# Kernel optimization log

Measured on AMD Instinct MI355X. Metric: run time of the kernel, lower is better.

The kernel has to match this reference:

```python
import jax, jax.numpy as jnp
import numpy as np

THRESHOLD = 0.05

def binarize101(w, threshold):
    # Ternary quantization to {-1, 0, +1}: zero inside the dead-zone [-thr, thr].
    pos = (w > threshold).astype(w.dtype)
    neg = (w < -threshold).astype(w.dtype)
    return pos - neg

def setup_inputs() -> dict:
    key = jax.random.key(0)
    k1, k2, k3 = jax.random.split(key, 3)
    x = jax.random.normal(k1, (8192, 4096), dtype=jnp.float32)
    weight = jax.random.normal(k2, (4096, 4096), dtype=jnp.float32)
    bias = jax.random.normal(k3, (4096,), dtype=jnp.float32)
    return {"x": x, "weight": weight, "bias": bias}

def reference(x, weight, bias):
    wb = binarize101(weight, THRESHOLD)
    # F.linear: x @ wb.T + bias ; x: [N, in], weight: [out, in] -> [N, out]
    return jnp.einsum('ni,oi->no', x, wb) + bias
```

## Files before the change

### kernel.cpp

```cpp
#include <hip/hip_runtime.h>

typedef float floatx16 __attribute__((ext_vector_type(16)));
typedef __bf16 bf16x8 __attribute__((ext_vector_type(8)));
using u16 = unsigned short;
using u32 = unsigned int;

#define GLOBAL_AS __attribute__((address_space(1)))
#define LDS_AS    __attribute__((address_space(3)))

__device__ __forceinline__ u32 rne_bf16(float f) {
  u32 u = __float_as_uint(f);
  return (u + 0x7FFFu + ((u >> 16) & 1u)) >> 16;
}

__global__ __launch_bounds__(256) void cvt_x_perm(const float* __restrict__ x,
                                                  u16* __restrict__ xb, int K) {
  __shared__ u16 sm[16384];
  const int tid = threadIdx.x;
  const int Kt = K >> 6;
  const int pn = blockIdx.x / Kt, tt = blockIdx.x % Kt;
  const float* src = x + (size_t)pn * 256 * K + tt * 64;
#pragma unroll
  for (int j = 0; j < 16; ++j) {
    const int fc = j * 256 + tid;
    const int row = fc >> 4, kl4 = fc & 15;
    const float4 v = *(const float4*)(src + (size_t)row * K + kl4 * 4);
    uint2 o;
    o.x = rne_bf16(v.x) | (rne_bf16(v.y) << 16);
    o.y = rne_bf16(v.z) | (rne_bf16(v.w) << 16);
    const int gi = row >> 5, rowin = row & 31;
    const int ks = kl4 >> 2;
    const int lane = rowin + 32 * ((kl4 >> 1) & 1);
    const int e4 = (kl4 & 1) * 4;
    *(uint2*)(sm + gi * 2048 + ks * 512 + lane * 8 + e4) = o;
  }
  __syncthreads();
  u16* dst = xb + (size_t)pn * 256 * K + (size_t)tt * 16384;
#pragma unroll
  for (int j = 0; j < 8; ++j) {
    const int o = (j * 256 + tid) * 8;
    *(uint4*)(dst + o) = *(const uint4*)(sm + o);
  }
}

__global__ __launch_bounds__(256) void quant_w_perm(const float* __restrict__ w,
                                                    u16* __restrict__ wb, int K) {
  __shared__ u16 sm[16384];
  const int tid = threadIdx.x;
  const int Kt = K >> 6;
  const int pn = blockIdx.x / Kt, tt = blockIdx.x % Kt;
  const float* src = w + (size_t)pn * 256 * K + tt * 64;
#pragma unroll
  for (int j = 0; j < 16; ++j) {
    const int fc = j * 256 + tid;
    const int row = fc >> 4, kl4 = fc & 15;
    const float4 v = *(const float4*)(src + (size_t)row * K + kl4 * 4);
    float vv[4] = {v.x, v.y, v.z, v.w};
    u32 r[4];
#pragma unroll
    for (int e = 0; e < 4; ++e)
      r[e] = (vv[e] > 0.05f) ? 0x3F80u : ((vv[e] < -0.05f) ? 0xBF80u : 0u);
    uint2 o;
    o.x = r[0] | (r[1] << 16);
    o.y = r[2] | (r[3] << 16);
    const int gi = row >> 5, rowin = row & 31;
    const int ks = kl4 >> 2;
    const int lane = rowin + 32 * ((kl4 >> 1) & 1);
    const int e4 = (kl4 & 1) * 4;
    *(uint2*)(sm + gi * 2048 + ks * 512 + lane * 8 + e4) = o;
  }
  __syncthreads();
  u16* dst = wb + (size_t)pn * 256 * K + (size_t)tt * 16384;
#pragma unroll
  for (int j = 0; j < 8; ++j) {
    const int o = (j * 256 + tid) * 8;
    *(uint4*)(dst + o) = *(const uint4*)(sm + o);
  }
}

__global__ __launch_bounds__(512, 2) void gemm_bin_m201d(
    const u16* __restrict__ Ap, const u16* __restrict__ Bp,
    const float* __restrict__ bias, float* __restrict__ C,
    int M, int N, int K) {
  __shared__ u16 lds[65536];

  const int tid = threadIdx.x;
  const int w = tid >> 6, l = tid & 63;
  const int wr = w >> 2, wc = w & 3;

  const int nbn = N >> 8;
  int wg = blockIdx.x;
  const int nwg = gridDim.x;
  if ((nwg & 7) == 0) wg = (wg & 7) * (nwg >> 3) + (wg >> 3);
  const int bm = wg / nbn, bn = wg % nbn;

  const int T = K >> 6;

  const u16* const Abase = Ap + (size_t)bm * ((size_t)K << 8) + tid * 8;
  const u16* const Bbase = Bp + (size_t)bn * ((size_t)K << 8) + tid * 8;

  const u16* const afp0 = lds + wr * 8192 + l * 8;
  const u16* const bfp0 = lds + 16384 + wc * 4096 + l * 8;

  floatx16 acc[4][2] = {};
  bf16x8 af[8], bflo[4], bfhi[4];

#define GLOAD(gptr, u16off)                                                    \
  __builtin_amdgcn_global_load_lds((const GLOBAL_AS void*)(gptr),              \
                                   (LDS_AS void*)(lds + (u16off)), 16, 0, 0)
#define BARRIER __builtin_amdgcn_s_barrier()
#define LGKM0  do { asm volatile("s_waitcnt lgkmcnt(0)" ::: "memory");         \
                    __builtin_amdgcn_sched_barrier(0); } while (0)

  GLOAD(Abase + 0 * 4096,      0 + tid * 8);
  GLOAD(Abase + 2 * 4096,   8192 + tid * 8);
  GLOAD(Bbase + 0 * 4096,  16384 + tid * 8);
  GLOAD(Bbase + 1 * 4096,  20480 + tid * 8);
  GLOAD(Bbase + 2 * 4096,  24576 + tid * 8);
  GLOAD(Bbase + 3 * 4096,  28672 + tid * 8);
  GLOAD(Abase + 1 * 4096,   4096 + tid * 8);
  GLOAD(Abase + 3 * 4096,  12288 + tid * 8);
  if (T > 1) {
    GLOAD(Abase + 16384 + 0 * 4096, 32768 + 0 + tid * 8);
    GLOAD(Abase + 16384 + 2 * 4096, 32768 + 8192 + tid * 8);
    GLOAD(Bbase + 16384 + 0 * 4096, 32768 + 16384 + tid * 8);
    GLOAD(Bbase + 16384 + 1 * 4096, 32768 + 20480 + tid * 8);
    GLOAD(Bbase + 16384 + 2 * 4096, 32768 + 24576 + tid * 8);
    GLOAD(Bbase + 16384 + 3 * 4096, 32768 + 28672 + tid * 8);
    asm volatile("s_waitcnt vmcnt(6)" ::: "memory");
  } else {
    asm volatile("s_waitcnt vmcnt(0)" ::: "memory");
  }
  BARRIER;

  for (int t = 0; t < T; ++t) {
    const int bufc = (t & 1) << 15;
    const int bufo = bufc ^ 32768;
    const bool st1 = (t + 1 < T);
    const bool st2 = (t + 2 < T);
    const size_t tn1 = (size_t)(t + 1) * 16384;
    const size_t tn2 = (size_t)(t + 2) * 16384;

    const u16* afp = afp0 + bufc;
    const u16* bfp = bfp0 + bufc;

#pragma unroll
    for (int m = 0; m < 2; ++m)
#pragma unroll
      for (int ks = 0; ks < 4; ++ks)
        af[m * 4 + ks] = *(const bf16x8*)(afp + m * 2048 + ks * 512);
#pragma unroll
    for (int ks = 0; ks < 4; ++ks) bflo[ks] = *(const bf16x8*)(bfp + ks * 512);
    if (st1) {
      GLOAD(Abase + tn1 + 1 * 4096, bufo + 4096 + tid * 8);
      GLOAD(Abase + tn1 + 3 * 4096, bufo + 12288 + tid * 8);
    }
    asm volatile("s_waitcnt lgkmcnt(8)" ::: "memory");
    BARRIER;
    LGKM0;
    __builtin_amdgcn_s_setprio(1);
#pragma unroll
    for (int ks = 0; ks < 4; ++ks)
#pragma unroll
      for (int m = 0; m < 2; ++m)
        acc[m][0] = __builtin_amdgcn_mfma_f32_32x32x16_bf16(
            af[m * 4 + ks], bflo[ks], acc[m][0], 0, 0, 0);
    __builtin_amdgcn_s_setprio(0);
    BARRIER;

#pragma unroll
    for (int ks = 0; ks < 4; ++ks) bfhi[ks] = *(const bf16x8*)(bfp + 2048 + ks * 512);
    if (st2) {
      GLOAD(Abase + tn2 + 0 * 4096, bufc + 0 + tid * 8);
      GLOAD(Abase + tn2 + 2 * 4096, bufc + 8192 + tid * 8);
    }
    BARRIER;
    LGKM0;
    __builtin_amdgcn_s_setprio(1);
#pragma unroll
    for (int ks = 0; ks < 4; ++ks)
#pragma unroll
      for (int m = 0; m < 2; ++m)
        acc[m][1] = __builtin_amdgcn_mfma_f32_32x32x16_bf16(
            af[m * 4 + ks], bfhi[ks], acc[m][1], 0, 0, 0);
    __builtin_amdgcn_s_setprio(0);
    BARRIER;

#pragma unroll
    for (int m = 0; m < 2; ++m)
#pragma unroll
      for (int ks = 0; ks < 4; ++ks)
        af[m * 4 + ks] = *(const bf16x8*)(afp + 4096 + m * 2048 + ks * 512);
    if (st2) {
      GLOAD(Bbase + tn2 + 0 * 4096, bufc + 16384 + tid * 8);
      GLOAD(Bbase + tn2 + 1 * 4096, bufc + 20480 + tid * 8);
    }
    asm volatile("s_waitcnt lgkmcnt(4)" ::: "memory");
    BARRIER;
    LGKM0;
    __builtin_amdgcn_s_setprio(1);
#pragma unroll
    for (int ks = 0; ks < 4; ++ks)
#pragma unroll
      for (int m = 0; m < 2; ++m)
        acc[2 + m][0] = __builtin_amdgcn_mfma_f32_32x32x16_bf16(
            af[m * 4 + ks], bflo[ks], acc[2 + m][0], 0, 0, 0);
    __builtin_amdgcn_s_setprio(0);
    BARRIER;

    if (st2) {
      GLOAD(Bbase + tn2 + 2 * 4096, bufc + 24576 + tid * 8);
      GLOAD(Bbase + tn2 + 3 * 4096, bufc + 28672 + tid * 8);
    }
    BARRIER;
    __builtin_amdgcn_s_setprio(1);
#pragma unroll
    for (int ks = 0; ks < 4; ++ks)
#pragma unroll
      for (int m = 0; m < 2; ++m)
        acc[2 + m][1] = __builtin_amdgcn_mfma_f32_32x32x16_bf16(
            af[m * 4 + ks], bfhi[ks], acc[2 + m][1], 0, 0, 0);
    __builtin_amdgcn_s_setprio(0);
    if (st2) asm volatile("s_waitcnt vmcnt(6)" ::: "memory");
    else     asm volatile("s_waitcnt vmcnt(0)" ::: "memory");
    BARRIER;
  }
#undef GLOAD
#undef BARRIER
#undef LGKM0

  const int colq = l & 31;
  const int hi4 = (l >> 5) * 4;
#pragma unroll
  for (int m = 0; m < 4; ++m) {
    const int rowb = bm * 256 + wr * 128 + m * 32 + hi4;
#pragma unroll
    for (int n = 0; n < 2; ++n) {
      const int col = bn * 256 + wc * 64 + n * 32 + colq;
      const float bv = bias[col];
      float* cp = C + (size_t)rowb * N + col;
#pragma unroll
      for (int q = 0; q < 16; ++q) {
        const int dr = (q & 3) + 8 * (q >> 2);
        cp[(size_t)dr * N] = acc[m][n][q] + bv;
      }
    }
  }
}

__global__ void gemm_naive_kernel(const float* __restrict__ x, const float* __restrict__ wgt,
                                  const float* __restrict__ bias, float* __restrict__ out,
                                  int M, int N, int K) {
  long long idx = (long long)blockIdx.x * blockDim.x + threadIdx.x;
  if (idx >= (long long)M * N) return;
  int o = (int)(idx % N);
  int m = (int)(idx / N);
  const float* xr = x + (size_t)m * K;
  const float* wr = wgt + (size_t)o * K;
  float s = 0.f;
  for (int i = 0; i < K; ++i) {
    float wv = wr[i];
    float t = (wv > 0.05f) ? 1.f : ((wv < -0.05f) ? -1.f : 0.f);
    s = fmaf(xr[i], t, s);
  }
  out[idx] = s + bias[o];
}

extern "C" void kernel_launch(void* const* d_in, const int* in_sizes, int n_in,
                              void* d_out, int out_size, void* d_ws, size_t ws_size,
                              hipStream_t stream) {
  const float* x    = (const float*)d_in[0];
  const float* wgt  = (const float*)d_in[1];
  const float* bias = (const float*)d_in[2];
  float* out = (float*)d_out;

  const int N = in_sizes[2];
  const int K = in_sizes[1] / N;
  const int M = in_sizes[0] / K;

  const size_t need = ((size_t)M * K + (size_t)N * K) * sizeof(u16);
  if (ws_size >= need && (M % 256 == 0) && (N % 256 == 0) && (K % 64 == 0) && K >= 192) {
    u16* xb = (u16*)d_ws;
    u16* wb = xb + (size_t)M * K;
    const int Kt = K / 64;
    cvt_x_perm<<<(M / 256) * Kt, 256, 0, stream>>>(x, xb, K);
    quant_w_perm<<<(N / 256) * Kt, 256, 0, stream>>>(wgt, wb, K);
    const int grid = (M / 256) * (N / 256);
    gemm_bin_m201d<<<grid, 512, 0, stream>>>(xb, wb, bias, out, M, N, K);
  } else {
    const long long total = (long long)M * N;
    gemm_naive_kernel<<<(unsigned)((total + 255) / 256), 256, 0, stream>>>(x, wgt, bias, out, M, N, K);
  }
}
```

Measured before the change: 286.4 us.

## Replace interleaved 3-stage barrier pipeline with simple double-buffered prefetch

Restructures the GEMM main loop. Instead of splitting the next-next tile's global-to-LDS loads across four barrier-separated MFMA phases, it issues the whole next tile at the start of each iteration into the other buffer. All LDS fragment reads for the current tile (with an extra af2 register set) complete before the MFMAs, and there is a single vmcnt(0)+barrier per iteration. This removes most intra-iteration barriers, at the cost of a shallower prefetch distance (one tile instead of effectively two), more VGPR pressure, and a full vmcnt(0) stall at each iteration end.

```diff
diff --git a/kernel.cpp b/kernel.cpp
--- a/kernel.cpp
+++ b/kernel.cpp
@@ -78,7 +78,7 @@
   }
 }
 
-__global__ __launch_bounds__(512, 2) void gemm_bin_m201d(
+__global__ __launch_bounds__(512, 2) void gemm_bin_flow(
     const u16* __restrict__ Ap, const u16* __restrict__ Bp,
     const float* __restrict__ bias, float* __restrict__ C,
     int M, int N, int K) {
@@ -103,43 +103,34 @@
   const u16* const bfp0 = lds + 16384 + wc * 4096 + l * 8;
 
   floatx16 acc[4][2] = {};
-  bf16x8 af[8], bflo[4], bfhi[4];
+  bf16x8 af[8], af2[8], bflo[4], bfhi[4];
 
 #define GLOAD(gptr, u16off)                                                    \
   __builtin_amdgcn_global_load_lds((const GLOBAL_AS void*)(gptr),              \
                                    (LDS_AS void*)(lds + (u16off)), 16, 0, 0)
-#define BARRIER __builtin_amdgcn_s_barrier()
-#define LGKM0  do { asm volatile("s_waitcnt lgkmcnt(0)" ::: "memory");         \
-                    __builtin_amdgcn_sched_barrier(0); } while (0)
-
-  GLOAD(Abase + 0 * 4096,      0 + tid * 8);
-  GLOAD(Abase + 2 * 4096,   8192 + tid * 8);
-  GLOAD(Bbase + 0 * 4096,  16384 + tid * 8);
-  GLOAD(Bbase + 1 * 4096,  20480 + tid * 8);
-  GLOAD(Bbase + 2 * 4096,  24576 + tid * 8);
-  GLOAD(Bbase + 3 * 4096,  28672 + tid * 8);
-  GLOAD(Abase + 1 * 4096,   4096 + tid * 8);
-  GLOAD(Abase + 3 * 4096,  12288 + tid * 8);
-  if (T > 1) {
-    GLOAD(Abase + 16384 + 0 * 4096, 32768 + 0 + tid * 8);
-    GLOAD(Abase + 16384 + 2 * 4096, 32768 + 8192 + tid * 8);
-    GLOAD(Bbase + 16384 + 0 * 4096, 32768 + 16384 + tid * 8);
-    GLOAD(Bbase + 16384 + 1 * 4096, 32768 + 20480 + tid * 8);
-    GLOAD(Bbase + 16384 + 2 * 4096, 32768 + 24576 + tid * 8);
-    GLOAD(Bbase + 16384 + 3 * 4096, 32768 + 28672 + tid * 8);
-    asm volatile("s_waitcnt vmcnt(6)" ::: "memory");
-  } else {
-    asm volatile("s_waitcnt vmcnt(0)" ::: "memory");
-  }
-  BARRIER;
+#define STAGE8(tt, bufdst)                                                     \
+  {                                                                            \
+    const size_t tb_ = (size_t)(tt) * 16384;                                   \
+    GLOAD(Abase + tb_ + 0 * 4096, (bufdst) + 0 + tid * 8);                     \
+    GLOAD(Abase + tb_ + 1 * 4096, (bufdst) + 4096 + tid * 8);                  \
+    GLOAD(Abase + tb_ + 2 * 4096, (bufdst) + 8192 + tid * 8);                  \
+    GLOAD(Abase + tb_ + 3 * 4096, (bufdst) + 12288 + tid * 8);                 \
+    GLOAD(Bbase + tb_ + 0 * 4096, (bufdst) + 16384 + tid * 8);                 \
+    GLOAD(Bbase + tb_ + 1 * 4096, (bufdst) + 20480 + tid * 8);                 \
+    GLOAD(Bbase + tb_ + 2 * 4096, (bufdst) + 24576 + tid * 8);                 \
+    GLOAD(Bbase + tb_ + 3 * 4096, (bufdst) + 28672 + tid * 8);                 \
+  }
+
+  STAGE8(0, 0)
+  asm volatile("s_waitcnt vmcnt(0)" ::: "memory");
+  __builtin_amdgcn_s_barrier();
 
   for (int t = 0; t < T; ++t) {
     const int bufc = (t & 1) << 15;
     const int bufo = bufc ^ 32768;
     const bool st1 = (t + 1 < T);
-    const bool st2 = (t + 2 < T);
-    const size_t tn1 = (size_t)(t + 1) * 16384;
-    const size_t tn2 = (size_t)(t + 2) * 16384;
+
+    if (st1) STAGE8(t + 1, bufo)
 
     const u16* afp = afp0 + bufc;
     const u16* bfp = bfp0 + bufc;
@@ -151,13 +142,11 @@
         af[m * 4 + ks] = *(const bf16x8*)(afp + m * 2048 + ks * 512);
 #pragma unroll
     for (int ks = 0; ks < 4; ++ks) bflo[ks] = *(const bf16x8*)(bfp + ks * 512);
-    if (st1) {
-      GLOAD(Abase + tn1 + 1 * 4096, bufo + 4096 + tid * 8);
-      GLOAD(Abase + tn1 + 3 * 4096, bufo + 12288 + tid * 8);
-    }
-    asm volatile("s_waitcnt lgkmcnt(8)" ::: "memory");
-    BARRIER;
-    LGKM0;
+#pragma unroll
+    for (int ks = 0; ks < 4; ++ks) bfhi[ks] = *(const bf16x8*)(bfp + 2048 + ks * 512);
+
+    asm volatile("s_waitcnt lgkmcnt(4)" ::: "memory");
+    __builtin_amdgcn_sched_barrier(0);
     __builtin_amdgcn_s_setprio(1);
 #pragma unroll
     for (int ks = 0; ks < 4; ++ks)
@@ -166,16 +155,15 @@
         acc[m][0] = __builtin_amdgcn_mfma_f32_32x32x16_bf16(
             af[m * 4 + ks], bflo[ks], acc[m][0], 0, 0, 0);
     __builtin_amdgcn_s_setprio(0);
-    BARRIER;
-
-#pragma unroll
-    for (int ks = 0; ks < 4; ++ks) bfhi[ks] = *(const bf16x8*)(bfp + 2048 + ks * 512);
-    if (st2) {
-      GLOAD(Abase + tn2 + 0 * 4096, bufc + 0 + tid * 8);
-      GLOAD(Abase + tn2 + 2 * 4096, bufc + 8192 + tid * 8);
-    }
-    BARRIER;
-    LGKM0;
+
+#pragma unroll
+    for (int m = 0; m < 2; ++m)
+#pragma unroll
+      for (int ks = 0; ks < 4; ++ks)
+        af2[m * 4 + ks] = *(const bf16x8*)(afp + 4096 + m * 2048 + ks * 512);
+
+    asm volatile("s_waitcnt lgkmcnt(8)" ::: "memory");
+    __builtin_amdgcn_sched_barrier(0);
     __builtin_amdgcn_s_setprio(1);
 #pragma unroll
     for (int ks = 0; ks < 4; ++ks)
@@ -184,50 +172,31 @@
         acc[m][1] = __builtin_amdgcn_mfma_f32_32x32x16_bf16(
             af[m * 4 + ks], bfhi[ks], acc[m][1], 0, 0, 0);
     __builtin_amdgcn_s_setprio(0);
-    BARRIER;
-
-#pragma unroll
-    for (int m = 0; m < 2; ++m)
-#pragma unroll
-      for (int ks = 0; ks < 4; ++ks)
-        af[m * 4 + ks] = *(const bf16x8*)(afp + 4096 + m * 2048 + ks * 512);
-    if (st2) {
-      GLOAD(Bbase + tn2 + 0 * 4096, bufc + 16384 + tid * 8);
-      GLOAD(Bbase + tn2 + 1 * 4096, bufc + 20480 + tid * 8);
+
+    asm volatile("s_waitcnt lgkmcnt(0)" ::: "memory");
+    __builtin_amdgcn_sched_barrier(0);
+    __builtin_amdgcn_s_setprio(1);
+#pragma unroll
+    for (int ks = 0; ks < 4; ++ks)
+#pragma unroll
+      for (int m = 0; m < 2; ++m)
+        acc[2 + m][0] = __builtin_amdgcn_mfma_f32_32x32x16_bf16(
+            af2[m * 4 + ks], bflo[ks], acc[2 + m][0], 0, 0, 0);
+#pragma unroll
+    for (int ks = 0; ks < 4; ++ks)
+#pragma unroll
+      for (int m = 0; m < 2; ++m)
+        acc[2 + m][1] = __builtin_amdgcn_mfma_f32_32x32x16_bf16(
+            af2[m * 4 + ks], bfhi[ks], acc[2 + m][1], 0, 0, 0);
+    __builtin_amdgcn_s_setprio(0);
+
+    if (st1) {
+      asm volatile("s_waitcnt vmcnt(0)" ::: "memory");
+      __builtin_amdgcn_s_barrier();
     }
-    asm volatile("s_waitcnt lgkmcnt(4)" ::: "memory");
-    BARRIER;
-    LGKM0;
-    __builtin_amdgcn_s_setprio(1);
-#pragma unroll
-    for (int ks = 0; ks < 4; ++ks)
-#pragma unroll
-      for (int m = 0; m < 2; ++m)
-        acc[2 + m][0] = __builtin_amdgcn_mfma_f32_32x32x16_bf16(
-            af[m * 4 + ks], bflo[ks], acc[2 + m][0], 0, 0, 0);
-    __builtin_amdgcn_s_setprio(0);
-    BARRIER;
-
-    if (st2) {
-      GLOAD(Bbase + tn2 + 2 * 4096, bufc + 24576 + tid * 8);
-      GLOAD(Bbase + tn2 + 3 * 4096, bufc + 28672 + tid * 8);
-    }
-    BARRIER;
-    __builtin_amdgcn_s_setprio(1);
-#pragma unroll
-    for (int ks = 0; ks < 4; ++ks)
-#pragma unroll
-      for (int m = 0; m < 2; ++m)
-        acc[2 + m][1] = __builtin_amdgcn_mfma_f32_32x32x16_bf16(
-            af[m * 4 + ks], bfhi[ks], acc[2 + m][1], 0, 0, 0);
-    __builtin_amdgcn_s_setprio(0);
-    if (st2) asm volatile("s_waitcnt vmcnt(6)" ::: "memory");
-    else     asm volatile("s_waitcnt vmcnt(0)" ::: "memory");
-    BARRIER;
-  }
+  }
+#undef STAGE8
 #undef GLOAD
-#undef BARRIER
-#undef LGKM0
 
   const int colq = l & 31;
   const int hi4 = (l >> 5) * 4;
@@ -286,7 +255,7 @@
     cvt_x_perm<<<(M / 256) * Kt, 256, 0, stream>>>(x, xb, K);
     quant_w_perm<<<(N / 256) * Kt, 256, 0, stream>>>(wgt, wb, K);
     const int grid = (M / 256) * (N / 256);
-    gemm_bin_m201d<<<grid, 512, 0, stream>>>(xb, wb, bias, out, M, N, K);
+    gemm_bin_flow<<<grid, 512, 0, stream>>>(xb, wb, bias, out, M, N, K);
   } else {
     const long long total = (long long)M * N;
     gemm_naive_kernel<<<(unsigned)((total + 255) / 256), 256, 0, stream>>>(x, wgt, bias, out, M, N, K);
```

Result: no change. 290.5 us (+1.4%).

## Pack ternary weights to 2 bits and decode into LDS inside GEMM

Applied to the files above, without the earlier changes.

The weight quantization kernel now emits 2-bit codes per ternary value instead of bf16, packed in the permuted MFMA layout. The GEMM loads the packed words with regular global loads into registers and decodes them into bf16 in LDS, replacing the direct global-to-LDS B tile loads. This cuts weight workspace traffic by a factor of eight and shrinks the quantization write. The cost is extra ALU decode work and LDS stores inside the main loop, plus a rearranged barrier and waitcnt schedule.

```diff
diff --git a/kernel.cpp b/kernel.cpp
--- a/kernel.cpp
+++ b/kernel.cpp
@@ -4,6 +4,7 @@
 typedef __bf16 bf16x8 __attribute__((ext_vector_type(8)));
 using u16 = unsigned short;
 using u32 = unsigned int;
+using u64 = unsigned long long;
 
 #define GLOBAL_AS __attribute__((address_space(1)))
 #define LDS_AS    __attribute__((address_space(3)))
@@ -43,42 +44,61 @@
   }
 }
 
-__global__ __launch_bounds__(256) void quant_w_perm(const float* __restrict__ w,
-                                                    u16* __restrict__ wb, int K) {
-  __shared__ u16 sm[16384];
+__global__ __launch_bounds__(512) void quant_w_pack2(const float* __restrict__ w,
+                                                     u16* __restrict__ wb, int K) {
+  __shared__ unsigned char cb[16384];
   const int tid = threadIdx.x;
   const int Kt = K >> 6;
   const int pn = blockIdx.x / Kt, tt = blockIdx.x % Kt;
   const float* src = w + (size_t)pn * 256 * K + tt * 64;
 #pragma unroll
-  for (int j = 0; j < 16; ++j) {
-    const int fc = j * 256 + tid;
+  for (int j = 0; j < 8; ++j) {
+    const int fc = j * 512 + tid;
     const int row = fc >> 4, kl4 = fc & 15;
     const float4 v = *(const float4*)(src + (size_t)row * K + kl4 * 4);
     float vv[4] = {v.x, v.y, v.z, v.w};
-    u32 r[4];
-#pragma unroll
-    for (int e = 0; e < 4; ++e)
-      r[e] = (vv[e] > 0.05f) ? 0x3F80u : ((vv[e] < -0.05f) ? 0xBF80u : 0u);
-    uint2 o;
-    o.x = r[0] | (r[1] << 16);
-    o.y = r[2] | (r[3] << 16);
-    const int gi = row >> 5, rowin = row & 31;
-    const int ks = kl4 >> 2;
-    const int lane = rowin + 32 * ((kl4 >> 1) & 1);
-    const int e4 = (kl4 & 1) * 4;
-    *(uint2*)(sm + gi * 2048 + ks * 512 + lane * 8 + e4) = o;
+    u32 c4 = 0;
+#pragma unroll
+    for (int e = 0; e < 4; ++e) {
+      u32 c = (vv[e] > 0.05f) ? 1u : ((vv[e] < -0.05f) ? 3u : 0u);
+      c4 |= c << (8 * e);
+    }
+    *(u32*)(cb + row * 64 + kl4 * 4) = c4;
   }
   __syncthreads();
-  u16* dst = wb + (size_t)pn * 256 * K + (size_t)tt * 16384;
-#pragma unroll
-  for (int j = 0; j < 8; ++j) {
-    const int o = (j * 256 + tid) * 8;
-    *(uint4*)(dst + o) = *(const uint4*)(sm + o);
-  }
-}
-
-__global__ __launch_bounds__(512, 2) void gemm_bin_m201d(
+  const int ni = tid >> 6, ks = (tid >> 4) & 3, lb = 4 * (tid & 15);
+  u32 half[4];
+#pragma unroll
+  for (int g = 0; g < 4; ++g) {
+    const int l_loc = lb + g;
+    const int n_loc = ni * 32 + (l_loc & 31);
+    const int kb = ks * 16 + (l_loc >> 5) * 8;
+    const u64 b = *(const u64*)(cb + n_loc * 64 + kb);
+    u32 h = 0;
+#pragma unroll
+    for (int e = 0; e < 8; ++e) h |= (u32)((b >> (8 * e)) & 3u) << (2 * e);
+    half[g] = h;
+  }
+  uint2 pk;
+  pk.x = half[0] | (half[1] << 16);
+  pk.y = half[2] | (half[3] << 16);
+  *(uint2*)(wb + ((size_t)(pn * Kt + tt) * 512 + tid) * 4) = pk;
+}
+
+__device__ __forceinline__ uint4 dec4(u32 word, int sh) {
+  uint4 o;
+  u32* p = (u32*)&o;
+#pragma unroll
+  for (int i = 0; i < 4; ++i) {
+    const u32 x = (word >> (sh + 4 * i)) & 0xFu;
+    const u32 lo = (x & 1u) * 0x3F80u | ((x & 2u) << 14);
+    const u32 hi = ((x >> 2) & 1u) * 0x3F80u | ((x & 8u) << 12);
+    p[i] = lo | (hi << 16);
+  }
+  return o;
+}
+
+__global__ __launch_bounds__(512, 2) void gemm_bin_pk2(
     const u16* __restrict__ Ap, const u16* __restrict__ Bp,
     const float* __restrict__ bias, float* __restrict__ C,
     int M, int N, int K) {
@@ -97,13 +117,15 @@
   const int T = K >> 6;
 
   const u16* const Abase = Ap + (size_t)bm * ((size_t)K << 8) + tid * 8;
-  const u16* const Bbase = Bp + (size_t)bn * ((size_t)K << 8) + tid * 8;
+  const u16* const pkbase = Bp + (size_t)bn * T * 2048 + tid * 4;
 
   const u16* const afp0 = lds + wr * 8192 + l * 8;
   const u16* const bfp0 = lds + 16384 + wc * 4096 + l * 8;
+  const int bwr = 16384 + tid * 32;
 
   floatx16 acc[4][2] = {};
   bf16x8 af[8], bflo[4], bfhi[4];
+  uint2 pk;
 
 #define GLOAD(gptr, u16off)                                                    \
   __builtin_amdgcn_global_load_lds((const GLOBAL_AS void*)(gptr),              \
@@ -113,24 +135,28 @@
                     __builtin_amdgcn_sched_barrier(0); } while (0)
 
   GLOAD(Abase + 0 * 4096,      0 + tid * 8);
+  GLOAD(Abase + 1 * 4096,   4096 + tid * 8);
   GLOAD(Abase + 2 * 4096,   8192 + tid * 8);
-  GLOAD(Bbase + 0 * 4096,  16384 + tid * 8);
-  GLOAD(Bbase + 1 * 4096,  20480 + tid * 8);
-  GLOAD(Bbase + 2 * 4096,  24576 + tid * 8);
-  GLOAD(Bbase + 3 * 4096,  28672 + tid * 8);
-  GLOAD(Abase + 1 * 4096,   4096 + tid * 8);
   GLOAD(Abase + 3 * 4096,  12288 + tid * 8);
   if (T > 1) {
     GLOAD(Abase + 16384 + 0 * 4096, 32768 + 0 + tid * 8);
     GLOAD(Abase + 16384 + 2 * 4096, 32768 + 8192 + tid * 8);
-    GLOAD(Bbase + 16384 + 0 * 4096, 32768 + 16384 + tid * 8);
-    GLOAD(Bbase + 16384 + 1 * 4096, 32768 + 20480 + tid * 8);
-    GLOAD(Bbase + 16384 + 2 * 4096, 32768 + 24576 + tid * 8);
-    GLOAD(Bbase + 16384 + 3 * 4096, 32768 + 28672 + tid * 8);
-    asm volatile("s_waitcnt vmcnt(6)" ::: "memory");
-  } else {
-    asm volatile("s_waitcnt vmcnt(0)" ::: "memory");
-  }
+  }
+  {
+    uint2 p0 = *(const uint2*)(pkbase);
+    *(uint4*)(lds + bwr + 0)  = dec4(p0.x, 0);
+    *(uint4*)(lds + bwr + 8)  = dec4(p0.x, 16);
+    *(uint4*)(lds + bwr + 16) = dec4(p0.y, 0);
+    *(uint4*)(lds + bwr + 24) = dec4(p0.y, 16);
+    if (T > 1) {
+      uint2 p1 = *(const uint2*)(pkbase + 2048);
+      *(uint4*)(lds + 32768 + bwr + 0)  = dec4(p1.x, 0);
+      *(uint4*)(lds + 32768 + bwr + 8)  = dec4(p1.x, 16);
+      *(uint4*)(lds + 32768 + bwr + 16) = dec4(p1.y, 0);
+      *(uint4*)(lds + 32768 + bwr + 24) = dec4(p1.y, 16);
+    }
+  }
+  asm volatile("s_waitcnt vmcnt(0) lgkmcnt(0)" ::: "memory");
   BARRIER;
 
   for (int t = 0; t < T; ++t) {
@@ -155,6 +181,7 @@
       GLOAD(Abase + tn1 + 1 * 4096, bufo + 4096 + tid * 8);
       GLOAD(Abase + tn1 + 3 * 4096, bufo + 12288 + tid * 8);
     }
+    if (st2) pk = *(const uint2*)(pkbase + tn2 / 8);
     asm volatile("s_waitcnt lgkmcnt(8)" ::: "memory");
     BARRIER;
     LGKM0;
@@ -191,10 +218,6 @@
 #pragma unroll
       for (int ks = 0; ks < 4; ++ks)
         af[m * 4 + ks] = *(const bf16x8*)(afp + 4096 + m * 2048 + ks * 512);
-    if (st2) {
-      GLOAD(Bbase + tn2 + 0 * 4096, bufc + 16384 + tid * 8);
-      GLOAD(Bbase + tn2 + 1 * 4096, bufc + 20480 + tid * 8);
-    }
     asm volatile("s_waitcnt lgkmcnt(4)" ::: "memory");
     BARRIER;
     LGKM0;
@@ -206,13 +229,12 @@
         acc[2 + m][0] = __builtin_amdgcn_mfma_f32_32x32x16_bf16(
             af[m * 4 + ks], bflo[ks], acc[2 + m][0], 0, 0, 0);
     __builtin_amdgcn_s_setprio(0);
-    BARRIER;
-
     if (st2) {
-      GLOAD(Bbase + tn2 + 2 * 4096, bufc + 24576 + tid * 8);
-      GLOAD(Bbase + tn2 + 3 * 4096, bufc + 28672 + tid * 8);
-    }
-    BARRIER;
+      *(uint4*)(lds + bufc + bwr - 16384 + 16384 + 0) = dec4(pk.x, 0);
+      *(uint4*)(lds + bufc + bwr + 8) = dec4(pk.x, 16);
+    }
+    BARRIER;
+
     __builtin_amdgcn_s_setprio(1);
 #pragma unroll
     for (int ks = 0; ks < 4; ++ks)
@@ -221,9 +243,15 @@
         acc[2 + m][1] = __builtin_amdgcn_mfma_f32_32x32x16_bf16(
             af[m * 4 + ks], bfhi[ks], acc[2 + m][1], 0, 0, 0);
     __builtin_amdgcn_s_setprio(0);
-    if (st2) asm volatile("s_waitcnt vmcnt(6)" ::: "memory");
-    else     asm volatile("s_waitcnt vmcnt(0)" ::: "memory");
-    BARRIER;
+    if (st2) {
+      *(uint4*)(lds + bufc + bwr + 16) = dec4(pk.y, 0);
+      *(uint4*)(lds + bufc + bwr + 24) = dec4(pk.y, 16);
+    }
+    if (st1) {
+      if (st2) asm volatile("s_waitcnt vmcnt(2) lgkmcnt(0)" ::: "memory");
+      else     asm volatile("s_waitcnt vmcnt(0) lgkmcnt(0)" ::: "memory");
+      BARRIER;
+    }
   }
 #undef GLOAD
 #undef BARRIER
@@ -278,15 +306,15 @@
   const int K = in_sizes[1] / N;
   const int M = in_sizes[0] / K;
 
-  const size_t need = ((size_t)M * K + (size_t)N * K) * sizeof(u16);
-  if (ws_size >= need && (M % 256 == 0) && (N % 256 == 0) && (K % 64 == 0) && K >= 192) {
+  const size_t need = (size_t)M * K * 2 + (size_t)N * K / 4;
+  if (ws_size >= need && (M % 256 == 0) && (N % 256 == 0) && (K % 64 == 0) && K >= 256) {
     u16* xb = (u16*)d_ws;
     u16* wb = xb + (size_t)M * K;
     const int Kt = K / 64;
     cvt_x_perm<<<(M / 256) * Kt, 256, 0, stream>>>(x, xb, K);
-    quant_w_perm<<<(N / 256) * Kt, 256, 0, stream>>>(wgt, wb, K);
+    quant_w_pack2<<<(N / 256) * Kt, 512, 0, stream>>>(wgt, wb, K);
     const int grid = (M / 256) * (N / 256);
-    gemm_bin_m201d<<<grid, 512, 0, stream>>>(xb, wb, bias, out, M, N, K);
+    gemm_bin_pk2<<<grid, 512, 0, stream>>>(xb, wb, bias, out, M, N, K);
   } else {
     const long long total = (long long)M * N;
     gemm_naive_kernel<<<(unsigned)((total + 255) / 256), 256, 0, stream>>>(x, wgt, bias, out, M, N, K);
```

After: 361.6 us. 26.3% more time.
